# Kernel tuning notes

Measured on AMD Instinct MI355X. Metric: run time of the kernel, lower is better.

## Reference

```python
import jax, jax.numpy as jnp
import numpy as np
from jax import lax

B_, NCH, T = 128, 22, 1000
F1, F2 = 8, 16
BN_EPS = 1e-5


def _conv(x, w, b, pad, groups=1):
    y = lax.conv_general_dilated(x, w, (1, 1), pad,
                                 dimension_numbers=('NCHW', 'OIHW', 'NCHW'),
                                 feature_group_count=groups)
    return y if b is None else y + b[None, :, None, None]


def _bn(x, g, b):
    # eval-mode BatchNorm2d with running_mean=0, running_var=1
    return x * (g / np.sqrt(1.0 + BN_EPS))[None, :, None, None] + b[None, :, None, None]


def _avgpool(x, w, s):
    y = lax.reduce_window(x, 0.0, lax.add, (1, 1, 1, w), (1, 1, 1, s), 'VALID')
    return y / w


def _ln(x, g, b):
    m = x.mean(-1, keepdims=True)
    v = ((x - m) ** 2).mean(-1, keepdims=True)
    return (x - m) * lax.rsqrt(v + 1e-5) * g + b


def _enc_layer(h, qw, qb, pw, pb, f1w, f1b, f2w, f2b, g1, b1, g2, b2):
    # h: (S, N, E). Torch TransformerEncoderLayer default is seq-first, so axis 0
    # (the STDCNN batch dim) is attended over -- faithfully reproduced here.
    S, N, E = h.shape
    H = 8
    hd = E // H
    q, k, v = jnp.split(h @ qw.T + qb, 3, axis=-1)
    q = q.reshape(S, N, H, hd)
    k = k.reshape(S, N, H, hd)
    v = v.reshape(S, N, H, hd)
    att = jax.nn.softmax(jnp.einsum('snhd,tnhd->nhst', q, k) / np.sqrt(hd), axis=-1)
    o = jnp.einsum('nhst,tnhd->snhd', att, v).reshape(S, N, E) @ pw.T + pb
    h = _ln(h + o, g1, b1)
    ff = jax.nn.relu(h @ f1w.T + f1b) @ f2w.T + f2b
    return _ln(h + ff, g2, b2)


def setup_inputs() -> dict:
    key = jax.random.key(0)
    ks = iter(jax.random.split(key, 48))

    def nrm(shape, s=0.1):
        return jax.random.normal(next(ks), shape, jnp.float32) * s

    inp = dict(
        x=jax.random.normal(next(ks), (B_, 1, NCH, T), jnp.float32),
        w_spec1=nrm((F1, 1, 1, 125)), b_spec1=nrm((F1,)),
        w_spec2=nrm((F1, 1, 1, 30)), b_spec2=nrm((F1,)),
        g_bn1=1.0 + nrm((F1,)), b_bn1=nrm((F1,)),
        g_bn2=1.0 + nrm((F1,)), b_bn2=nrm((F1,)),
        w_sp1a=nrm((F2, 1, NCH, 1)),
        g_bn3=1.0 + nrm((F2,)), b_bn3=nrm((F2,)),
        w_sp1b=nrm((F2, F2, 1, 1)), b_sp1b=nrm((F2,)),
        g_bn4=1.0 + nrm((F2,)), b_bn4=nrm((F2,)),
        w_sp2=nrm((F2, F1, NCH, 1)), b_sp2=nrm((F2,)),
        g_bn5=1.0 + nrm((F2,)), b_bn5=nrm((F2,)),
        A=jnp.eye(F2, dtype=jnp.float32) + nrm((F2, F2), 0.01),
        Bm=nrm((F2, F2)),
        Cm=jnp.eye(F2, dtype=jnp.float32) + nrm((F2, F2), 0.01),
        qkv_w=nrm((2, 3 * F2, F2)), qkv_b=nrm((2, 3 * F2)),
        proj_w=nrm((2, F2, F2)), proj_b=nrm((2, F2)),
        ff1_w=nrm((2, 64, F2)), ff1_b=nrm((2, 64)),
        ff2_w=nrm((2, F2, 64)), ff2_b=nrm((2, F2)),
        ln1_g=jnp.ones((2, F2), jnp.float32), ln1_b=jnp.zeros((2, F2), jnp.float32),
        ln2_g=jnp.ones((2, F2), jnp.float32), ln2_b=jnp.zeros((2, F2), jnp.float32),
    )
    return inp


def reference(x, w_spec1, b_spec1, w_spec2, b_spec2, g_bn1, b_bn1, g_bn2, b_bn2,
              w_sp1a, g_bn3, b_bn3, w_sp1b, b_sp1b, g_bn4, b_bn4,
              w_sp2, b_sp2, g_bn5, b_bn5, A, Bm, Cm,
              qkv_w, qkv_b, proj_w, proj_b, ff1_w, ff1_b, ff2_w, ff2_b,
              ln1_g, ln1_b, ln2_g, ln2_b):
    # spectral branches (torch 'same' padding: k=125 -> (62,62); k=30 -> (14,15))
    x1 = _bn(_conv(x, w_spec1, b_spec1, [(0, 0), (62, 62)]), g_bn1, b_bn1)
    x2 = _bn(_conv(x, w_spec2, b_spec2, [(0, 0), (14, 15)]), g_bn2, b_bn2)
    # spatial branch 1 (dropout is identity in eval)
    s1 = jax.nn.elu(_bn(_conv(x1, w_sp1a, None, 'VALID', groups=F1), g_bn3, b_bn3))
    s1 = jax.nn.elu(_bn(_conv(s1, w_sp1b, b_sp1b, 'VALID'), g_bn4, b_bn4))
    s1 = _avgpool(s1, 32, 32)                                   # (B,16,1,31)
    # spatial branch 2: square -> avgpool -> log(clamp)
    s2 = _bn(_conv(x2, w_sp2, b_sp2, 'VALID'), g_bn5, b_bn5)
    s2 = jnp.log(jnp.clip(_avgpool(jnp.square(s2), 75, 25), 1e-6))  # (B,16,1,38)
    xc = jnp.concatenate([s1, s2], axis=3)                       # (B,16,1,69)
    Bn, Cc, H2, W2 = xc.shape
    seq = xc.reshape(Bn, Cc, H2 * W2).transpose(0, 2, 1)         # (B,L,16)

    # linear SSM recurrence (torch for-loop -> lax.scan)
    def step(state, xt):
        state = state @ A + xt @ Bm.T
        return state, state @ Cm.T

    _, outs = lax.scan(step, jnp.zeros((Bn, F2), seq.dtype), seq.transpose(1, 0, 2))
    h = outs.transpose(1, 0, 2)                                  # (B,L,16)

    for l in range(2):
        h = _enc_layer(h, qkv_w[l], qkv_b[l], proj_w[l], proj_b[l],
                       ff1_w[l], ff1_b[l], ff2_w[l], ff2_b[l],
                       ln1_g[l], ln1_b[l], ln2_g[l], ln2_b[l])

    return h.reshape(Bn, W2, 1, Cc).transpose(0, 3, 2, 1)        # (B,16,1,69)
```

## Files before the change

kernel.cpp:

```cpp
#include <hip/hip_runtime.h>
#include <hip/hip_bf16.h>
#include <math.h>

#define BBATCH 128
#define NCHAN  22
#define TLEN   1000
#define F1C    8
#define F2C    16
#define L1W    31
#define L2W    38
#define LSEQ   69
#define EDIM   16
#define NHEAD  8
#define FFDIM  64

#define C_SA   0
#define C_BA   16
#define C_BC2  32
#define C_AW   4144
#define C_AW1  (C_AW + 5632)
#define C_TOTAL (C_AW1 + 22528)

#define OFF_CONST 0
#define OFF_CHNK  40960
#define OFF_SEQ   (OFF_CHNK + 81920)
#define OFF_STB   (OFF_SEQ + 141312)
#define OFF_HBUF  (OFF_STB + 141312)

typedef __attribute__((ext_vector_type(8))) short bf16x8;
typedef __attribute__((ext_vector_type(4))) float f32x4;

static __device__ __forceinline__ unsigned short f2bf(float f) {
    unsigned u = __float_as_uint(f);
    unsigned r = (u + 0x7FFFu + ((u >> 16) & 1u)) >> 16;
    return (unsigned short)r;
}

#define SWZ(v, imm) __int_as_float(__builtin_amdgcn_ds_swizzle(__float_as_int(v), imm))
#define MV16(dst, sv, W) do { \
    float p0=SWZ(sv,0x010)*W[0],  p1=SWZ(sv,0x030)*W[1],  \
          p2=SWZ(sv,0x050)*W[2],  p3=SWZ(sv,0x070)*W[3],  \
          p4=SWZ(sv,0x090)*W[4],  p5=SWZ(sv,0x0B0)*W[5],  \
          p6=SWZ(sv,0x0D0)*W[6],  p7=SWZ(sv,0x0F0)*W[7],  \
          p8=SWZ(sv,0x110)*W[8],  p9=SWZ(sv,0x130)*W[9],  \
          p10=SWZ(sv,0x150)*W[10],p11=SWZ(sv,0x170)*W[11],\
          p12=SWZ(sv,0x190)*W[12],p13=SWZ(sv,0x1B0)*W[13],\
          p14=SWZ(sv,0x1D0)*W[14],p15=SWZ(sv,0x1F0)*W[15];\
    dst = (((p0+p1)+(p2+p3))+((p4+p5)+(p6+p7))) + (((p8+p9)+(p10+p11))+((p12+p13)+(p14+p15))); \
} while(0)

__global__ void k_setup(const float* __restrict__ wsp1a, const float* __restrict__ b_spec1,
                        const float* __restrict__ g_bn1, const float* __restrict__ b_bn1,
                        const float* __restrict__ g_bn3, const float* __restrict__ b_bn3,
                        const float* __restrict__ w_spec2, const float* __restrict__ b_spec2,
                        const float* __restrict__ g_bn2, const float* __restrict__ b_bn2,
                        const float* __restrict__ w_sp2, const float* __restrict__ b_sp2,
                        const float* __restrict__ g_bn5, const float* __restrict__ b_bn5,
                        const float* __restrict__ w_spec1,
                        float* __restrict__ consts)
{
    int tid = threadIdx.x;
    int gb = blockIdx.x;
    int NG = gridDim.x;
    int gid = gb*256 + tid;
    float rbn = rsqrtf(1.0f + 1e-5f);
    if (gb == 0 && tid < 16) {
        int c2 = tid, c1 = c2 >> 1;
        float wsum = 0.f;
        for (int h = 0; h < NCHAN; h++) wsum += wsp1a[c2*NCHAN + h];
        float s1b = g_bn1[c1] * rbn;
        float s3  = g_bn3[c2] * rbn;
        float C1  = (s1b * b_spec1[c1] + b_bn1[c1]) * wsum;
        consts[C_SA + c2] = s3 * s1b;
        consts[C_BA + c2] = s3 * C1 + b_bn3[c2];
        float s5 = g_bn5[c2] * rbn;
        float acc = b_sp2[c2];
        for (int cc = 0; cc < F1C; cc++) {
            float s2b = g_bn2[cc] * rbn;
            float cb  = s2b * b_spec2[cc] + b_bn2[cc];
            float wsh = 0.f;
            for (int h = 0; h < NCHAN; h++) wsh += w_sp2[(c2*F1C + cc)*NCHAN + h];
            acc += wsh * cb;
        }
        consts[C_BC2 + c2] = s5 * acc + b_bn5[c2];
    }
    unsigned* aw = (unsigned*)&consts[C_AW];
    for (int idx = gid; idx < 22*64*4; idx += 256*NG) {
        int r = idx & 3;
        int l = (idx >> 2) & 63;
        int c = idx >> 8;
        int m = l & 15;
        int k0 = ((l >> 4) << 3) + 2*r;
        float s5 = g_bn5[m] * rbn;
        float w0 = 0.f, w1 = 0.f;
        for (int cc = 0; cc < F1C; cc++) {
            float f = w_sp2[(m*F1C + cc)*NCHAN + c] * (g_bn2[cc] * rbn);
            if (k0 < 30)     w0 += f * w_spec2[cc*30 + k0];
            if (k0 + 1 < 30) w1 += f * w_spec2[cc*30 + k0 + 1];
        }
        w0 *= s5; w1 *= s5;
        aw[idx] = (unsigned)f2bf(w0) | ((unsigned)f2bf(w1) << 16);
    }
    unsigned* aw1 = (unsigned*)&consts[C_AW1];
    for (int idx = gid; idx < 22*4*64*4; idx += 256*NG) {
        int r = idx & 3;
        int l = (idx >> 2) & 63;
        int kk = (idx >> 8) & 3;
        int c = idx >> 10;
        int m = l & 15;
        int klocal = ((l >> 4) << 3) + 2*r;
        int tap0 = kk*32 + klocal;
        float sa = (g_bn3[m] * rbn) * (g_bn1[m >> 1] * rbn);
        float base = sa * wsp1a[m*NCHAN + c];
        float w0 = (tap0     < 125) ? base * w_spec1[(m >> 1)*125 + tap0]     : 0.f;
        float w1 = (tap0 + 1 < 125) ? base * w_spec1[(m >> 1)*125 + tap0 + 1] : 0.f;
        aw1[idx] = (unsigned)f2bf(w0) | ((unsigned)f2bf(w1) << 16);
    }
}

#define PB1 384
#define NW1 (NCHAN*PB1)
#define PS1 257
#define PB2 288
#define SQP2 257
#define FRONT_SM 12560

__device__ __forceinline__ void b1mm_body(float* smem, int bid,
    const float* __restrict__ x, const float* __restrict__ consts,
    const float* __restrict__ w_sp1b, const float* __restrict__ b_sp1b,
    const float* __restrict__ g_bn4, const float* __restrict__ b_bn4,
    float* __restrict__ seq)
{
    unsigned short* xs = (unsigned short*)smem;
    float* sq = smem + 8448;
    const uint4* __restrict__ awg = (const uint4*)&consts[C_AW1];
    int q = bid & 3, b = bid >> 2;
    int t0 = q * 256;
    int tid = threadIdx.x;

    for (int idx = tid; idx < NW1; idx += 256) {
        int h = idx / PB1, e = idx - h*PB1;
        int t = t0 - 62 + e;
        const float* xr = x + (b*NCHAN + h)*TLEN;
        float v0 = ((unsigned)t < 1000u && e < 380) ? xr[t] : 0.f;
        float v1 = ((unsigned)(t+1) < 1000u && e < 380) ? xr[t+1] : 0.f;
        xs[idx] = f2bf(v0);
        xs[NW1 + idx] = f2bf(v1);
    }
    __syncthreads();

    int lane = tid & 63, wid = tid >> 6;
    int tp = lane & 15;
    int kb = (lane >> 4) << 3;
    int P = tp & 1;
    int tb0 = wid * 64;
    const unsigned short* xb = xs + P*NW1 + (tb0 + tp + kb - P);

    f32x4 a0 = {0.f,0.f,0.f,0.f};
    f32x4 a1 = a0, a2 = a0, a3 = a0;
    for (int c = 0; c < NCHAN; c++) {
#pragma unroll
        for (int kk = 0; kk < 4; kk++) {
            uint4 au = awg[(c*4 + kk)*64 + lane];
            union Ua { uint4 q; bf16x8 v; } A; A.q = au;
            const unsigned short* row = xb + c*PB1 + kk*32;
            union Uv { bf16x8 v; unsigned u[4]; };
            Uv B0, B1, B2, B3;
#pragma unroll
            for (int r = 0; r < 4; r++) {
                B0.u[r] = *(const unsigned*)(row + 2*r);
                B1.u[r] = *(const unsigned*)(row + 16 + 2*r);
                B2.u[r] = *(const unsigned*)(row + 32 + 2*r);
                B3.u[r] = *(const unsigned*)(row + 48 + 2*r);
            }
            a0 = __builtin_amdgcn_mfma_f32_16x16x32_bf16(A.v, B0.v, a0, 0, 0, 0);
            a1 = __builtin_amdgcn_mfma_f32_16x16x32_bf16(A.v, B1.v, a1, 0, 0, 0);
            a2 = __builtin_amdgcn_mfma_f32_16x16x32_bf16(A.v, B2.v, a2, 0, 0, 0);
            a3 = __builtin_amdgcn_mfma_f32_16x16x32_bf16(A.v, B3.v, a3, 0, 0, 0);
        }
    }

    {
        int c2b = (lane >> 4) * 4;
        float ba[4];
#pragma unroll
        for (int r = 0; r < 4; r++) ba[r] = consts[C_BA + c2b + r];
#pragma unroll
        for (int r = 0; r < 4; r++) {
            float v, e;
            v = a0[r] + ba[r]; e = (v > 0.f) ? v : (expf(v) - 1.f);
            sq[(c2b+r)*PS1 + tb0 + tp +  0] = e;
            v = a1[r] + ba[r]; e = (v > 0.f) ? v : (expf(v) - 1.f);
            sq[(c2b+r)*PS1 + tb0 + tp + 16] = e;
            v = a2[r] + ba[r]; e = (v > 0.f) ? v : (expf(v) - 1.f);
            sq[(c2b+r)*PS1 + tb0 + tp + 32] = e;
            v = a3[r] + ba[r]; e = (v > 0.f) ? v : (expf(v) - 1.f);
            sq[(c2b+r)*PS1 + tb0 + tp + 48] = e;
        }
    }
    __syncthreads();

    {
        int u = tid;
        int w = 8*q + (u >> 5);
        float rbn = rsqrtf(1.0f + 1e-5f);
        float hv[16];
#pragma unroll
        for (int c = 0; c < 16; c++) hv[c] = sq[c*PS1 + u];
        float p[16];
#pragma unroll
        for (int c = 0; c < 16; c++) {
            float s = 0.f;
#pragma unroll
            for (int j = 0; j < 16; j++) s += w_sp1b[c*16 + j] * hv[j];
            float sc = g_bn4[c] * rbn;
            float a = sc * (s + b_sp1b[c]) + b_bn4[c];
            float g = (a > 0.f) ? a : (expf(a) - 1.f);
            g += __shfl_xor(g, 1, 64);
            g += __shfl_xor(g, 2, 64);
            g += __shfl_xor(g, 4, 64);
            g += __shfl_xor(g, 8, 64);
            g += __shfl_xor(g, 16, 64);
            p[c] = g;
        }
        if ((u & 31) == 0 && w < L1W) {
            float* sp = &seq[(b*LSEQ + w)*16];
#pragma unroll
            for (int i = 0; i < 4; i++)
                *(float4*)&sp[4*i] = make_float4(p[4*i]*(1.f/32.f), p[4*i+1]*(1.f/32.f),
                                                 p[4*i+2]*(1.f/32.f), p[4*i+3]*(1.f/32.f));
        }
    }
}

__device__ __forceinline__ void b2mm_body(float* smem, int bid,
    const float* __restrict__ x, const float* __restrict__ consts,
    float* __restrict__ chnk)
{
    unsigned short* xs = (unsigned short*)smem;
    float* sq = smem + 6336;
    const unsigned* __restrict__ awg = (const unsigned*)&consts[C_AW];
    int q = bid & 3, b = bid >> 2;
    int t0 = q * 250;
    int tid = threadIdx.x;

    for (int idx = tid; idx < NCHAN*PB2; idx += 256) {
        int h = idx / PB2, e = idx - h*PB2;
        int t = t0 - 14 + e;
        const float* xr = x + (b*NCHAN + h)*TLEN;
        float v0 = ((unsigned)t < 1000u) ? xr[t] : 0.f;
        float v1 = ((unsigned)(t+1) < 1000u) ? xr[t+1] : 0.f;
        xs[idx] = f2bf(v0);
        xs[NCHAN*PB2 + idx] = f2bf(v1);
    }
    __syncthreads();

    int lane = tid & 63, wid = tid >> 6;
    int tp = lane & 15;
    int kb = (lane >> 4) << 3;
    int P = tp & 1;
    int tb0 = wid * 64;
    const unsigned short* xb = xs + P*(NCHAN*PB2) + (tb0 + tp + kb - P);

    f32x4 a0 = {0.f,0.f,0.f,0.f};
    f32x4 a1 = a0, a2 = a0, a3 = a0;
    for (int c = 0; c < NCHAN; c++) {
        bf16x8 af = *(const bf16x8*)(awg + (c*64 + lane)*4);
        const unsigned short* row = xb + c*PB2;
        union Uv { bf16x8 v; unsigned u[4]; };
        Uv B0, B1, B2, B3;
#pragma unroll
        for (int r = 0; r < 4; r++) {
            B0.u[r] = *(const unsigned*)(row + 2*r);
            B1.u[r] = *(const unsigned*)(row + 16 + 2*r);
            B2.u[r] = *(const unsigned*)(row + 32 + 2*r);
            B3.u[r] = *(const unsigned*)(row + 48 + 2*r);
        }
        a0 = __builtin_amdgcn_mfma_f32_16x16x32_bf16(af, B0.v, a0, 0, 0, 0);
        a1 = __builtin_amdgcn_mfma_f32_16x16x32_bf16(af, B1.v, a1, 0, 0, 0);
        a2 = __builtin_amdgcn_mfma_f32_16x16x32_bf16(af, B2.v, a2, 0, 0, 0);
        a3 = __builtin_amdgcn_mfma_f32_16x16x32_bf16(af, B3.v, a3, 0, 0, 0);
    }

    {
        int c2b = (lane >> 4) * 4;
        float bc[4];
#pragma unroll
        for (int r = 0; r < 4; r++) bc[r] = consts[C_BC2 + c2b + r];
#pragma unroll
        for (int r = 0; r < 4; r++) {
            float v;
            v = a0[r] + bc[r]; sq[(c2b+r)*SQP2 + tb0 + tp +  0] = v*v;
            v = a1[r] + bc[r]; sq[(c2b+r)*SQP2 + tb0 + tp + 16] = v*v;
            v = a2[r] + bc[r]; sq[(c2b+r)*SQP2 + tb0 + tp + 32] = v*v;
            v = a3[r] + bc[r]; sq[(c2b+r)*SQP2 + tb0 + tp + 48] = v*v;
        }
    }
    __syncthreads();

    if (tid < 160) {
        int c2 = tid / 10, ch = tid % 10;
        const float* s = &sq[c2*SQP2 + ch*25];
        float acc2 = 0.f;
#pragma unroll
        for (int i = 0; i < 25; i++) acc2 += s[i];
        chnk[(b*16 + c2)*40 + q*10 + ch] = acc2;
    }
}

__global__ __launch_bounds__(256, 2)
void k_front(const float* __restrict__ x,
             const float* __restrict__ consts,
             const float* __restrict__ w_sp1b, const float* __restrict__ b_sp1b,
             const float* __restrict__ g_bn4, const float* __restrict__ b_bn4,
             float* __restrict__ seq, float* __restrict__ chnk)
{
    __shared__ __align__(16) float smem[FRONT_SM];
    int bid = blockIdx.x;
    if (bid < BBATCH*4) {
        b1mm_body(smem, bid, x, consts, w_sp1b, b_sp1b, g_bn4, b_bn4, seq);
    } else {
        b2mm_body(smem, bid - BBATCH*4, x, consts, chnk);
    }
}

__global__ __launch_bounds__(64, 1)
void k_ssm(const float* __restrict__ seq, const float* __restrict__ chnk,
           const float* __restrict__ Amat, const float* __restrict__ Bmat,
           float* __restrict__ stbuf)
{
    int tid = threadIdx.x;
    int j = tid & 15;
    int b = blockIdx.x * 4 + (tid >> 4);

    float Acol[16], Brow[16];
#pragma unroll
    for (int i = 0; i < 16; i++) {
        Acol[i] = Amat[i*16 + j];
        Brow[i] = Bmat[j*16 + i];
    }

    float xv[LSEQ];
#pragma unroll
    for (int l = 0; l < 31; l++) xv[l] = seq[(b*LSEQ + l)*16 + j];
    {
        float cp[40];
        const float4* cpp = (const float4*)(chnk + (b*16 + j)*40);
#pragma unroll
        for (int i = 0; i < 10; i++) {
            float4 v = cpp[i];
            cp[4*i]=v.x; cp[4*i+1]=v.y; cp[4*i+2]=v.z; cp[4*i+3]=v.w;
        }
#pragma unroll
        for (int w = 0; w < 38; w++) {
            float m = (cp[w] + cp[w+1] + cp[w+2]) * (1.f/75.f);
            xv[31 + w] = logf(fmaxf(m, 1e-6f));
        }
    }

#pragma unroll
    for (int l = 0; l < LSEQ; l++) {
        float u;
        MV16(u, xv[l], Brow);
        xv[l] = u;
    }

    float st = 0.f;
#pragma unroll
    for (int l = 0; l < LSEQ; l++) {
        float nv;
        MV16(nv, st, Acol);
        st = nv + xv[l];
        stbuf[(l*BBATCH + b)*16 + j] = st;
    }
}

#define KVS2 38
__global__ __launch_bounds__(256, 2)
void k_tfl(const float* __restrict__ hin, const float* __restrict__ Cmat, int applyC,
           const float* __restrict__ qw, const float* __restrict__ qb,
           const float* __restrict__ pw, const float* __restrict__ pb,
           const float* __restrict__ f1w, const float* __restrict__ f1b,
           const float* __restrict__ f2w, const float* __restrict__ f2b,
           const float* __restrict__ g1, const float* __restrict__ b1,
           const float* __restrict__ g2, const float* __restrict__ b2,
           float* __restrict__ hout, float* __restrict__ fout, int writeFinal)
{
    __shared__ __align__(16) float sm[2176 + 128*KVS2 + 576 + 544 + 7*544 + 2048 + 64];
    float* h_l  = sm;
    float* kvq  = sm + 2176;
    float* qbuf = sm + 2176 + 128*KVS2;
    float* olds = qbuf + 576;
    float* ffp  = olds + 544;
    float* f1l  = ffp + 7*544;
    float* f2l  = f1l + 1024;
    float* f1bl = f2l + 1024;

    int tid = threadIdx.x;
    int rl = tid >> 3, hh = tid & 7;
    int n = blockIdx.x >> 2, q2 = blockIdx.x & 3;
    int s = q2*32 + rl;

    for (int i = tid; i < 1024; i += 256) { f1l[i] = f1w[i]; f2l[i] = f2w[i]; }
    if (tid < 64) f1bl[tid] = f1b[tid];

    {
        int r = tid >> 1, qd = tid & 1;
        if (applyC) {
            const float4* fr = (const float4*)(hin + (n*BBATCH + r)*16);
            float rv[16];
#pragma unroll
            for (int i = 0; i < 4; i++) {
                float4 a = fr[i];
                rv[4*i]=a.x; rv[4*i+1]=a.y; rv[4*i+2]=a.z; rv[4*i+3]=a.w;
            }
#pragma unroll
            for (int cq = 0; cq < 8; cq++) {
                int c = 8*qd + cq;
                float sum = 0.f;
#pragma unroll
                for (int i = 0; i < 16; i++) sum += rv[i] * Cmat[c*16 + i];
                h_l[r*17 + c] = sum;
            }
        } else {
            const float4* sr = (const float4*)(hin + (n*BBATCH + r)*16 + qd*8);
            float4 a0 = sr[0];
            float4 a1 = sr[1];
            h_l[r*17 + qd*8 + 0] = a0.x; h_l[r*17 + qd*8 + 1] = a0.y;
            h_l[r*17 + qd*8 + 2] = a0.z; h_l[r*17 + qd*8 + 3] = a0.w;
            h_l[r*17 + qd*8 + 4] = a1.x; h_l[r*17 + qd*8 + 5] = a1.y;
            h_l[r*17 + qd*8 + 6] = a1.z; h_l[r*17 + qd*8 + 7] = a1.w;
        }
    }
    __syncthreads();

    {
        int r2 = tid & 127;
        int ob = 16 + (tid >> 7) * 16;
        float hv[16];
#pragma unroll
        for (int c = 0; c < 16; c++) hv[c] = h_l[r2*17 + c];
#pragma unroll
        for (int oq = 0; oq < 16; oq++) {
            int o = ob + oq;
            float sum = qb[o];
#pragma unroll
            for (int c = 0; c < 16; c++) sum += qw[o*16 + c] * hv[c];
            kvq[r2*KVS2 + (o - 16)] = sum;
        }
        if (tid < 32) {
            int sr = q2*32 + tid;
            float hq[16];
#pragma unroll
            for (int c = 0; c < 16; c++) hq[c] = h_l[sr*17 + c];
#pragma unroll
            for (int o = 0; o < 16; o++) {
                float sum = qb[o];
#pragma unroll
                for (int c = 0; c < 16; c++) sum += qw[o*16 + c] * hq[c];
                qbuf[tid*18 + o] = sum;
            }
        }
    }
    __syncthreads();

    {
        const float SC = 1.0201941311775597f;
        float q0 = qbuf[rl*18 + 2*hh] * SC;
        float q1 = qbuf[rl*18 + 2*hh + 1] * SC;
        const float* kbase = &kvq[2*hh];
        float m0 = -1e30f, m1 = -1e30f, m2 = -1e30f, m3 = -1e30f;
#pragma unroll
        for (int tb = 0; tb < 128; tb += 4) {
            float2 k0 = *(const float2*)&kbase[(tb+0)*KVS2];
            float2 k1 = *(const float2*)&kbase[(tb+1)*KVS2];
            float2 k2 = *(const float2*)&kbase[(tb+2)*KVS2];
            float2 k3 = *(const float2*)&kbase[(tb+3)*KVS2];
            m0 = fmaxf(m0, q0*k0.x + q1*k0.y);
            m1 = fmaxf(m1, q0*k1.x + q1*k1.y);
            m2 = fmaxf(m2, q0*k2.x + q1*k2.y);
            m3 = fmaxf(m3, q0*k3.x + q1*k3.y);
        }
        float M = fmaxf(fmaxf(m0, m1), fmaxf(m2, m3));
        float su0 = 0.f, su1 = 0.f, su2 = 0.f, su3 = 0.f;
        float av0 = 0.f, av1 = 0.f, av2 = 0.f, av3 = 0.f;
        float bv0 = 0.f, bv1 = 0.f, bv2 = 0.f, bv3 = 0.f;
#pragma unroll
        for (int tb = 0; tb < 128; tb += 4) {
            float2 k0 = *(const float2*)&kbase[(tb+0)*KVS2];
            float2 k1 = *(const float2*)&kbase[(tb+1)*KVS2];
            float2 k2 = *(const float2*)&kbase[(tb+2)*KVS2];
            float2 k3 = *(const float2*)&kbase[(tb+3)*KVS2];
            float2 v0 = *(const float2*)&kbase[(tb+0)*KVS2 + 16];
            float2 v1 = *(const float2*)&kbase[(tb+1)*KVS2 + 16];
            float2 v2 = *(const float2*)&kbase[(tb+2)*KVS2 + 16];
            float2 v3 = *(const float2*)&kbase[(tb+3)*KVS2 + 16];
            float e0 = exp2f(q0*k0.x + q1*k0.y - M);
            float e1 = exp2f(q0*k1.x + q1*k1.y - M);
            float e2 = exp2f(q0*k2.x + q1*k2.y - M);
            float e3 = exp2f(q0*k3.x + q1*k3.y - M);
            su0 += e0; av0 += e0*v0.x; bv0 += e0*v0.y;
            su1 += e1; av1 += e1*v1.x; bv1 += e1*v1.y;
            su2 += e2; av2 += e2*v2.x; bv2 += e2*v2.y;
            su3 += e3; av3 += e3*v3.x; bv3 += e3*v3.y;
        }
        float su = (su0 + su1) + (su2 + su3);
        float av = (av0 + av1) + (av2 + av3);
        float bv = (bv0 + bv1) + (bv2 + bv3);
        float inv = 1.f / su;
        olds[rl*17 + 2*hh + 0] = av * inv;
        olds[rl*17 + 2*hh + 1] = bv * inv;
    }
    __syncthreads();

    {
        float rv[16], ov[16];
#pragma unroll
        for (int c = 0; c < 16; c++) { rv[c] = h_l[s*17 + c]; ov[c] = olds[rl*17 + c]; }
        float h1[16];
#pragma unroll
        for (int c = 0; c < 16; c++) {
            float p = pb[c];
#pragma unroll
            for (int j = 0; j < 16; j++) p += pw[c*16 + j] * ov[j];
            h1[c] = rv[c] + p;
        }
        float mn = 0.f;
#pragma unroll
        for (int c = 0; c < 16; c++) mn += h1[c];
        mn *= (1.f/16.f);
        float var = 0.f;
#pragma unroll
        for (int c = 0; c < 16; c++) { float d = h1[c] - mn; var += d*d; }
        var *= (1.f/16.f);
        float rs = rsqrtf(var + 1e-5f);
        float y[16];
#pragma unroll
        for (int c = 0; c < 16; c++) y[c] = (h1[c] - mn)*rs*g1[c] + b1[c];

        float t2[16];
#pragma unroll
        for (int c = 0; c < 16; c++) t2[c] = (hh == 0) ? f2b[c] : 0.f;
#pragma unroll
        for (int uq = 0; uq < 8; uq++) {
            int u = 8*hh + uq;
            float sv = f1bl[u];
#pragma unroll
            for (int c = 0; c < 16; c++) sv += f1l[u*16 + c] * y[c];
            sv = fmaxf(sv, 0.f);
#pragma unroll
            for (int c = 0; c < 16; c++) t2[c] += f2l[c*64 + u] * sv;
        }
        if (hh) {
#pragma unroll
            for (int c = 0; c < 16; c++) ffp[(hh-1)*544 + rl*17 + c] = t2[c];
        }
        __syncthreads();
        if (hh == 0) {
#pragma unroll
            for (int k = 0; k < 7; k++)
#pragma unroll
                for (int c = 0; c < 16; c++) t2[c] += ffp[k*544 + rl*17 + c];
            float h2[16];
#pragma unroll
            for (int c = 0; c < 16; c++) h2[c] = y[c] + t2[c];
            mn = 0.f;
#pragma unroll
            for (int c = 0; c < 16; c++) mn += h2[c];
            mn *= (1.f/16.f);
            var = 0.f;
#pragma unroll
            for (int c = 0; c < 16; c++) { float d = h2[c] - mn; var += d*d; }
            var *= (1.f/16.f);
            rs = rsqrtf(var + 1e-5f);
            if (writeFinal) {
#pragma unroll
                for (int c = 0; c < 16; c++)
                    fout[(s*16 + c)*LSEQ + n] = (h2[c] - mn)*rs*g2[c] + b2[c];
            } else {
                float z[16];
#pragma unroll
                for (int c = 0; c < 16; c++) z[c] = (h2[c] - mn)*rs*g2[c] + b2[c];
                float* hp = hout + (n*BBATCH + s)*16;
#pragma unroll
                for (int i = 0; i < 4; i++)
                    *(float4*)&hp[4*i] = make_float4(z[4*i], z[4*i+1], z[4*i+2], z[4*i+3]);
            }
        }
    }
}

extern "C" void kernel_launch(void* const* d_in, const int* in_sizes, int n_in,
                              void* d_out, int out_size, void* d_ws, size_t ws_size,
                              hipStream_t stream)
{
    const float* x       = (const float*)d_in[0];
    const float* w_spec1 = (const float*)d_in[1];
    const float* b_spec1 = (const float*)d_in[2];
    const float* w_spec2 = (const float*)d_in[3];
    const float* b_spec2 = (const float*)d_in[4];
    const float* g_bn1   = (const float*)d_in[5];
    const float* b_bn1   = (const float*)d_in[6];
    const float* g_bn2   = (const float*)d_in[7];
    const float* b_bn2   = (const float*)d_in[8];
    const float* w_sp1a  = (const float*)d_in[9];
    const float* g_bn3   = (const float*)d_in[10];
    const float* b_bn3   = (const float*)d_in[11];
    const float* w_sp1b  = (const float*)d_in[12];
    const float* b_sp1b  = (const float*)d_in[13];
    const float* g_bn4   = (const float*)d_in[14];
    const float* b_bn4   = (const float*)d_in[15];
    const float* w_sp2   = (const float*)d_in[16];
    const float* b_sp2   = (const float*)d_in[17];
    const float* g_bn5   = (const float*)d_in[18];
    const float* b_bn5   = (const float*)d_in[19];
    const float* Amat    = (const float*)d_in[20];
    const float* Bmat    = (const float*)d_in[21];
    const float* Cmat    = (const float*)d_in[22];
    const float* qkv_w   = (const float*)d_in[23];
    const float* qkv_b   = (const float*)d_in[24];
    const float* proj_w  = (const float*)d_in[25];
    const float* proj_b  = (const float*)d_in[26];
    const float* ff1_w   = (const float*)d_in[27];
    const float* ff1_b   = (const float*)d_in[28];
    const float* ff2_w   = (const float*)d_in[29];
    const float* ff2_b   = (const float*)d_in[30];
    const float* ln1_g   = (const float*)d_in[31];
    const float* ln1_b   = (const float*)d_in[32];
    const float* ln2_g   = (const float*)d_in[33];
    const float* ln2_b   = (const float*)d_in[34];

    float* ws  = (float*)d_ws;
    float* out = (float*)d_out;

    float* consts = ws + OFF_CONST;
    float* chnk   = ws + OFF_CHNK;
    float* seq    = ws + OFF_SEQ;
    float* stbuf  = ws + OFF_STB;
    float* hbuf   = ws + OFF_HBUF;

    k_setup<<<24, 256, 0, stream>>>(w_sp1a, b_spec1, g_bn1, b_bn1, g_bn3, b_bn3,
                                    w_spec2, b_spec2, g_bn2, b_bn2,
                                    w_sp2, b_sp2, g_bn5, b_bn5, w_spec1, consts);
    k_front<<<BBATCH*4 + BBATCH*4, 256, 0, stream>>>(x, consts,
        w_sp1b, b_sp1b, g_bn4, b_bn4, seq, chnk);
    k_ssm<<<BBATCH/4, 64, 0, stream>>>(seq, chnk, Amat, Bmat, stbuf);

    k_tfl<<<LSEQ*4, 256, 0, stream>>>(stbuf, Cmat, 1,
        qkv_w, qkv_b, proj_w, proj_b, ff1_w, ff1_b, ff2_w, ff2_b,
        ln1_g, ln1_b, ln2_g, ln2_b, hbuf, out, 0);
    k_tfl<<<LSEQ*4, 256, 0, stream>>>(hbuf, Cmat, 0,
        qkv_w + 768, qkv_b + 48, proj_w + 256, proj_b + 16,
        ff1_w + 1024, ff1_b + 64, ff2_w + 1024, ff2_b + 16,
        ln1_g + 16, ln1_b + 16, ln2_g + 16, ln2_b + 16, hbuf, out, 1);
}
```

Measured before the change: 117.0 us.

## Fuse both spatial branches into one front block sharing the staged input tile

```diff
diff --git a/kernel.cpp b/kernel.cpp
--- a/kernel.cpp
+++ b/kernel.cpp
@@ -118,34 +118,35 @@
     }
 }
 
-#define PB1 384
-#define NW1 (NCHAN*PB1)
-#define PS1 257
-#define PB2 288
-#define SQP2 257
+#define PB 384
+#define NW (NCHAN*PB)
+#define PS 257
 #define FRONT_SM 12560
 
-__device__ __forceinline__ void b1mm_body(float* smem, int bid,
-    const float* __restrict__ x, const float* __restrict__ consts,
-    const float* __restrict__ w_sp1b, const float* __restrict__ b_sp1b,
-    const float* __restrict__ g_bn4, const float* __restrict__ b_bn4,
-    float* __restrict__ seq)
+__global__ __launch_bounds__(256, 2)
+void k_front(const float* __restrict__ x,
+             const float* __restrict__ consts,
+             const float* __restrict__ w_sp1b, const float* __restrict__ b_sp1b,
+             const float* __restrict__ g_bn4, const float* __restrict__ b_bn4,
+             float* __restrict__ seq, float* __restrict__ chnk)
 {
+    __shared__ __align__(16) float smem[FRONT_SM];
     unsigned short* xs = (unsigned short*)smem;
     float* sq = smem + 8448;
-    const uint4* __restrict__ awg = (const uint4*)&consts[C_AW1];
+
+    int bid = blockIdx.x;
     int q = bid & 3, b = bid >> 2;
     int t0 = q * 256;
     int tid = threadIdx.x;
 
-    for (int idx = tid; idx < NW1; idx += 256) {
-        int h = idx / PB1, e = idx - h*PB1;
+    for (int idx = tid; idx < NW; idx += 256) {
+        int h = idx / PB, e = idx - h*PB;
         int t = t0 - 62 + e;
         const float* xr = x + (b*NCHAN + h)*TLEN;
         float v0 = ((unsigned)t < 1000u && e < 380) ? xr[t] : 0.f;
         float v1 = ((unsigned)(t+1) < 1000u && e < 380) ? xr[t+1] : 0.f;
         xs[idx] = f2bf(v0);
-        xs[NW1 + idx] = f2bf(v1);
+        xs[NW + idx] = f2bf(v1);
     }
     __syncthreads();
 
@@ -154,33 +155,33 @@
     int kb = (lane >> 4) << 3;
     int P = tp & 1;
     int tb0 = wid * 64;
-    const unsigned short* xb = xs + P*NW1 + (tb0 + tp + kb - P);
-
-    f32x4 a0 = {0.f,0.f,0.f,0.f};
-    f32x4 a1 = a0, a2 = a0, a3 = a0;
-    for (int c = 0; c < NCHAN; c++) {
-#pragma unroll
-        for (int kk = 0; kk < 4; kk++) {
-            uint4 au = awg[(c*4 + kk)*64 + lane];
-            union Ua { uint4 q; bf16x8 v; } A; A.q = au;
-            const unsigned short* row = xb + c*PB1 + kk*32;
-            union Uv { bf16x8 v; unsigned u[4]; };
-            Uv B0, B1, B2, B3;
-#pragma unroll
-            for (int r = 0; r < 4; r++) {
-                B0.u[r] = *(const unsigned*)(row + 2*r);
-                B1.u[r] = *(const unsigned*)(row + 16 + 2*r);
-                B2.u[r] = *(const unsigned*)(row + 32 + 2*r);
-                B3.u[r] = *(const unsigned*)(row + 48 + 2*r);
+
+    {
+        const uint4* __restrict__ awg = (const uint4*)&consts[C_AW1];
+        const unsigned short* xb = xs + P*NW + (tb0 + tp + kb - P);
+        f32x4 a0 = {0.f,0.f,0.f,0.f};
+        f32x4 a1 = a0, a2 = a0, a3 = a0;
+        for (int c = 0; c < NCHAN; c++) {
+#pragma unroll
+            for (int kk = 0; kk < 4; kk++) {
+                uint4 au = awg[(c*4 + kk)*64 + lane];
+                union Ua { uint4 qv; bf16x8 v; } A; A.qv = au;
+                const unsigned short* row = xb + c*PB + kk*32;
+                union Uv { bf16x8 v; unsigned u[4]; };
+                Uv B0, B1, B2, B3;
+#pragma unroll
+                for (int r = 0; r < 4; r++) {
+                    B0.u[r] = *(const unsigned*)(row + 2*r);
+                    B1.u[r] = *(const unsigned*)(row + 16 + 2*r);
+                    B2.u[r] = *(const unsigned*)(row + 32 + 2*r);
+                    B3.u[r] = *(const unsigned*)(row + 48 + 2*r);
+                }
+                a0 = __builtin_amdgcn_mfma_f32_16x16x32_bf16(A.v, B0.v, a0, 0, 0, 0);
+                a1 = __builtin_amdgcn_mfma_f32_16x16x32_bf16(A.v, B1.v, a1, 0, 0, 0);
+                a2 = __builtin_amdgcn_mfma_f32_16x16x32_bf16(A.v, B2.v, a2, 0, 0, 0);
+                a3 = __builtin_amdgcn_mfma_f32_16x16x32_bf16(A.v, B3.v, a3, 0, 0, 0);
             }
-            a0 = __builtin_amdgcn_mfma_f32_16x16x32_bf16(A.v, B0.v, a0, 0, 0, 0);
-            a1 = __builtin_amdgcn_mfma_f32_16x16x32_bf16(A.v, B1.v, a1, 0, 0, 0);
-            a2 = __builtin_amdgcn_mfma_f32_16x16x32_bf16(A.v, B2.v, a2, 0, 0, 0);
-            a3 = __builtin_amdgcn_mfma_f32_16x16x32_bf16(A.v, B3.v, a3, 0, 0, 0);
-        }
-    }
-
-    {
+        }
         int c2b = (lane >> 4) * 4;
         float ba[4];
 #pragma unroll
@@ -189,13 +190,13 @@
         for (int r = 0; r < 4; r++) {
             float v, e;
             v = a0[r] + ba[r]; e = (v > 0.f) ? v : (expf(v) - 1.f);
-            sq[(c2b+r)*PS1 + tb0 + tp +  0] = e;
+            sq[(c2b+r)*PS + tb0 + tp +  0] = e;
             v = a1[r] + ba[r]; e = (v > 0.f) ? v : (expf(v) - 1.f);
-            sq[(c2b+r)*PS1 + tb0 + tp + 16] = e;
+            sq[(c2b+r)*PS + tb0 + tp + 16] = e;
             v = a2[r] + ba[r]; e = (v > 0.f) ? v : (expf(v) - 1.f);
-            sq[(c2b+r)*PS1 + tb0 + tp + 32] = e;
+            sq[(c2b+r)*PS + tb0 + tp + 32] = e;
             v = a3[r] + ba[r]; e = (v > 0.f) ? v : (expf(v) - 1.f);
-            sq[(c2b+r)*PS1 + tb0 + tp + 48] = e;
+            sq[(c2b+r)*PS + tb0 + tp + 48] = e;
         }
     }
     __syncthreads();
@@ -206,7 +207,7 @@
         float rbn = rsqrtf(1.0f + 1e-5f);
         float hv[16];
 #pragma unroll
-        for (int c = 0; c < 16; c++) hv[c] = sq[c*PS1 + u];
+        for (int c = 0; c < 16; c++) hv[c] = sq[c*PS + u];
         float p[16];
 #pragma unroll
         for (int c = 0; c < 16; c++) {
@@ -231,58 +232,32 @@
                                                  p[4*i+2]*(1.f/32.f), p[4*i+3]*(1.f/32.f));
         }
     }
-}
-
-__device__ __forceinline__ void b2mm_body(float* smem, int bid,
-    const float* __restrict__ x, const float* __restrict__ consts,
-    float* __restrict__ chnk)
-{
-    unsigned short* xs = (unsigned short*)smem;
-    float* sq = smem + 6336;
-    const unsigned* __restrict__ awg = (const unsigned*)&consts[C_AW];
-    int q = bid & 3, b = bid >> 2;
-    int t0 = q * 250;
-    int tid = threadIdx.x;
-
-    for (int idx = tid; idx < NCHAN*PB2; idx += 256) {
-        int h = idx / PB2, e = idx - h*PB2;
-        int t = t0 - 14 + e;
-        const float* xr = x + (b*NCHAN + h)*TLEN;
-        float v0 = ((unsigned)t < 1000u) ? xr[t] : 0.f;
-        float v1 = ((unsigned)(t+1) < 1000u) ? xr[t+1] : 0.f;
-        xs[idx] = f2bf(v0);
-        xs[NCHAN*PB2 + idx] = f2bf(v1);
-    }
     __syncthreads();
 
-    int lane = tid & 63, wid = tid >> 6;
-    int tp = lane & 15;
-    int kb = (lane >> 4) << 3;
-    int P = tp & 1;
-    int tb0 = wid * 64;
-    const unsigned short* xb = xs + P*(NCHAN*PB2) + (tb0 + tp + kb - P);
-
-    f32x4 a0 = {0.f,0.f,0.f,0.f};
-    f32x4 a1 = a0, a2 = a0, a3 = a0;
-    for (int c = 0; c < NCHAN; c++) {
-        bf16x8 af = *(const bf16x8*)(awg + (c*64 + lane)*4);
-        const unsigned short* row = xb + c*PB2;
-        union Uv { bf16x8 v; unsigned u[4]; };
-        Uv B0, B1, B2, B3;
-#pragma unroll
-        for (int r = 0; r < 4; r++) {
-            B0.u[r] = *(const unsigned*)(row + 2*r);
-            B1.u[r] = *(const unsigned*)(row + 16 + 2*r);
-            B2.u[r] = *(const unsigned*)(row + 32 + 2*r);
-            B3.u[r] = *(const unsigned*)(row + 48 + 2*r);
-        }
-        a0 = __builtin_amdgcn_mfma_f32_16x16x32_bf16(af, B0.v, a0, 0, 0, 0);
-        a1 = __builtin_amdgcn_mfma_f32_16x16x32_bf16(af, B1.v, a1, 0, 0, 0);
-        a2 = __builtin_amdgcn_mfma_f32_16x16x32_bf16(af, B2.v, a2, 0, 0, 0);
-        a3 = __builtin_amdgcn_mfma_f32_16x16x32_bf16(af, B3.v, a3, 0, 0, 0);
-    }
-
-    {
+    {
+        const unsigned* __restrict__ awg = (const unsigned*)&consts[C_AW];
+        int off = 48 - 6*q;
+        const unsigned short* xb = xs + P*NW + (tb0 + tp + kb - P + off);
+        f32x4 a0 = {0.f,0.f,0.f,0.f};
+        f32x4 a1 = a0, a2 = a0, a3 = a0;
+        for (int c = 0; c < NCHAN; c++) {
+            bf16x8 af = *(const bf16x8*)(awg + (c*64 + lane)*4);
+            const unsigned short* row = xb + c*PB;
+            union Uv { bf16x8 v; unsigned u[4]; };
+            Uv B0, B1, B2, B3;
+#pragma unroll
+            for (int r = 0; r < 4; r++) {
+                B0.u[r] = *(const unsigned*)(row + 2*r);
+                B1.u[r] = *(const unsigned*)(row + 16 + 2*r);
+                B2.u[r] = *(const unsigned*)(row + 32 + 2*r);
+                B3.u[r] = *(const unsigned*)(row + 48 + 2*r);
+            }
+            a0 = __builtin_amdgcn_mfma_f32_16x16x32_bf16(af, B0.v, a0, 0, 0, 0);
+            a1 = __builtin_amdgcn_mfma_f32_16x16x32_bf16(af, B1.v, a1, 0, 0, 0);
+            a2 = __builtin_amdgcn_mfma_f32_16x16x32_bf16(af, B2.v, a2, 0, 0, 0);
+            a3 = __builtin_amdgcn_mfma_f32_16x16x32_bf16(af, B3.v, a3, 0, 0, 0);
+        }
+        __syncthreads();
         int c2b = (lane >> 4) * 4;
         float bc[4];
 #pragma unroll
@@ -290,37 +265,21 @@
 #pragma unroll
         for (int r = 0; r < 4; r++) {
             float v;
-            v = a0[r] + bc[r]; sq[(c2b+r)*SQP2 + tb0 + tp +  0] = v*v;
-            v = a1[r] + bc[r]; sq[(c2b+r)*SQP2 + tb0 + tp + 16] = v*v;
-            v = a2[r] + bc[r]; sq[(c2b+r)*SQP2 + tb0 + tp + 32] = v*v;
-            v = a3[r] + bc[r]; sq[(c2b+r)*SQP2 + tb0 + tp + 48] = v*v;
+            v = a0[r] + bc[r]; sq[(c2b+r)*PS + tb0 + tp +  0] = v*v;
+            v = a1[r] + bc[r]; sq[(c2b+r)*PS + tb0 + tp + 16] = v*v;
+            v = a2[r] + bc[r]; sq[(c2b+r)*PS + tb0 + tp + 32] = v*v;
+            v = a3[r] + bc[r]; sq[(c2b+r)*PS + tb0 + tp + 48] = v*v;
         }
     }
     __syncthreads();
 
     if (tid < 160) {
         int c2 = tid / 10, ch = tid % 10;
-        const float* s = &sq[c2*SQP2 + ch*25];
+        const float* s = &sq[c2*PS + ch*25];
         float acc2 = 0.f;
 #pragma unroll
         for (int i = 0; i < 25; i++) acc2 += s[i];
         chnk[(b*16 + c2)*40 + q*10 + ch] = acc2;
-    }
-}
-
-__global__ __launch_bounds__(256, 2)
-void k_front(const float* __restrict__ x,
-             const float* __restrict__ consts,
-             const float* __restrict__ w_sp1b, const float* __restrict__ b_sp1b,
-             const float* __restrict__ g_bn4, const float* __restrict__ b_bn4,
-             float* __restrict__ seq, float* __restrict__ chnk)
-{
-    __shared__ __align__(16) float smem[FRONT_SM];
-    int bid = blockIdx.x;
-    if (bid < BBATCH*4) {
-        b1mm_body(smem, bid, x, consts, w_sp1b, b_sp1b, g_bn4, b_bn4, seq);
-    } else {
-        b2mm_body(smem, bid - BBATCH*4, x, consts, chnk);
     }
 }
 
@@ -642,7 +601,7 @@
     k_setup<<<24, 256, 0, stream>>>(w_sp1a, b_spec1, g_bn1, b_bn1, g_bn3, b_bn3,
                                     w_spec2, b_spec2, g_bn2, b_bn2,
                                     w_sp2, b_sp2, g_bn5, b_bn5, w_spec1, consts);
-    k_front<<<BBATCH*4 + BBATCH*4, 256, 0, stream>>>(x, consts,
+    k_front<<<BBATCH*4, 256, 0, stream>>>(x, consts,
         w_sp1b, b_sp1b, g_bn4, b_bn4, seq, chnk);
     k_ssm<<<BBATCH/4, 64, 0, stream>>>(seq, chnk, Amat, Bmat, stbuf);
 
```

Measured after the change: 121.3 us. +3.7%, slower.
